# Performance work log

Hardware: AMD Instinct MI355X
Metric: run time of the kernel (lower is better)

Reference implementation:

```python
import jax, jax.numpy as jnp
import numpy as np

H = 128        # hidden_size == embed dim
HEADS = 8
HD = H // HEADS  # 16
OUT = 2


def _mlp(x, w1, b1, w2, b2, w3, b3):
    # build_mlps(2, [128, 64, 128], ret_before_act=True, without_norm=True)
    x = jax.nn.relu(x @ w1.T + b1)
    x = jax.nn.relu(x @ w2.T + b2)
    return x @ w3.T + b3


def _cross_attn(q, kv, mask, wq, bq, wk, bk, wv, bv, wo, bo):
    # q: [B, A, H] agent queries; kv: [B, M, H] map polylines; mask: [B, M] True = padded
    B, A, _ = q.shape
    M = kv.shape[1]
    qh = (q @ wq.T + bq).reshape(B, A, HEADS, HD)
    kh = (kv @ wk.T + bk).reshape(B, M, HEADS, HD)
    vh = (kv @ wv.T + bv).reshape(B, M, HEADS, HD)
    scores = jnp.einsum('bahd,bmhd->bham', qh, kh) * (1.0 / np.sqrt(HD))
    scores = jnp.where(mask[:, None, None, :], jnp.finfo(scores.dtype).min, scores)
    attn = jax.nn.softmax(scores, axis=-1)
    out = jnp.einsum('bham,bmhd->bahd', attn, vh).reshape(B, A, H)
    return out @ wo.T + bo


def _lstm_cell(x, h, c, avail, w_ih, w_hh, b_ih, b_hh):
    # standard torch LSTMCell math, masked update per agent availability
    gates = x @ w_ih.T + b_ih + h @ w_hh.T + b_hh
    i, f, g, o = jnp.split(gates, 4, axis=-1)
    c_new = jax.nn.sigmoid(f) * c + jax.nn.sigmoid(i) * jnp.tanh(g)
    h_new = jax.nn.sigmoid(o) * jnp.tanh(c_new)
    m = avail[..., None]
    return jnp.where(m, h_new, h), jnp.where(m, c_new, c)


def setup_inputs() -> dict:
    key = jax.random.key(0)
    B, A, M, T = 128, 64, 512, 80
    ks = jax.random.split(key, 32)
    p = lambda k, shape: (jax.random.normal(k, shape, dtype=jnp.float32) * 0.02)
    map_avails = jax.random.uniform(ks[5], (B, M)) > 0.2
    map_avails = map_avails.at[:, :8].set(True)  # guarantee non-empty attention rows
    return {
        'current_features': jax.random.normal(ks[0], (B, A, 2), dtype=jnp.float32),
        'current_availabilities': jnp.ones((B, A), dtype=bool),
        'hidden': jax.random.normal(ks[1], (B, A, H), dtype=jnp.float32),
        'context': jax.random.normal(ks[2], (B, A, H), dtype=jnp.float32),
        'map_embedding': jax.random.normal(ks[3], (B, M, H), dtype=jnp.float32),
        'map_avails': map_avails,
        'n_timesteps': T,
        # state encoder MLP: 2 -> 128 -> 64 -> 128
        'enc_w1': p(ks[6], (128, 2)),  'enc_b1': jnp.zeros((128,), jnp.float32),
        'enc_w2': p(ks[7], (64, 128)), 'enc_b2': jnp.zeros((64,), jnp.float32),
        'enc_w3': p(ks[8], (128, 64)), 'enc_b3': jnp.zeros((128,), jnp.float32),
        # cross-attention projections
        'wq': p(ks[9], (H, H)),  'bq': jnp.zeros((H,), jnp.float32),
        'wk': p(ks[10], (H, H)), 'bk': jnp.zeros((H,), jnp.float32),
        'wv': p(ks[11], (H, H)), 'bv': jnp.zeros((H,), jnp.float32),
        'wo': p(ks[12], (H, H)), 'bo': jnp.zeros((H,), jnp.float32),
        # LSTM cell (input 128, hidden 128)
        'w_ih': p(ks[13], (4 * H, H)), 'w_hh': p(ks[14], (4 * H, H)),
        'b_ih': jnp.zeros((4 * H,), jnp.float32), 'b_hh': jnp.zeros((4 * H,), jnp.float32),
        # output head
        'lin_w': p(ks[15], (OUT, H)), 'lin_b': jnp.zeros((OUT,), jnp.float32),
    }


def reference(current_features, current_availabilities, hidden, context,
              map_embedding, map_avails, n_timesteps,
              enc_w1, enc_b1, enc_w2, enc_b2, enc_w3, enc_b3,
              wq, bq, wk, bk, wv, bv, wo, bo,
              w_ih, w_hh, b_ih, b_hh, lin_w, lin_b):
    state0 = current_features[..., :2]
    cross_mask = ~map_avails

    def step(carry, _):
        state, h, c = carry
        e = _mlp(state, enc_w1, enc_b1, enc_w2, enc_b2, enc_w3, enc_b3)
        e = _cross_attn(e, map_embedding, cross_mask, wq, bq, wk, bk, wv, bv, wo, bo)
        h, c = _lstm_cell(e, h, c, current_availabilities, w_ih, w_hh, b_ih, b_hh)
        state = state + h @ lin_w.T + lin_b
        return (state, h, c), state

    _, ys = jax.lax.scan(step, (state0, hidden, context), None, length=n_timesteps)
    return jnp.moveaxis(ys, 0, 2)  # [B, A, T, 2]
```

## Files before the change

kernel.cpp:

```cpp
#include <hip/hip_runtime.h>
#include <cstdint>
#include <cstddef>


typedef short short8 __attribute__((ext_vector_type(8)));
typedef float f32x4 __attribute__((ext_vector_type(4)));

#define LOG2E 1.4426950408889634f
#define QSCALE 0.36067376022224085f

__device__ __forceinline__ unsigned short f2bf(float f) {
  union { float f; unsigned int u; } v; v.f = f;
  unsigned int u = v.u;
  return (unsigned short)((u + 0x7fffu + ((u >> 16) & 1u)) >> 16);
}
__device__ __forceinline__ unsigned cvtpk_bf16(float lo, float hi) {
  unsigned r;
  asm("v_cvt_pk_bf16_f32 %0, %1, %2" : "=v"(r) : "v"(lo), "v"(hi));
  return r;
}
__device__ __forceinline__ float fexp2(float x) {
  return __builtin_amdgcn_exp2f(x);
}
__device__ __forceinline__ float frcp(float x) {
  return __builtin_amdgcn_rcpf(x);
}
__device__ __forceinline__ float sigm(float x) {
  return frcp(1.f + fexp2(-LOG2E * x));
}
__device__ __forceinline__ float tanh_f(float x) {
  return 1.f - 2.f * frcp(1.f + fexp2(2.f * LOG2E * x));
}
__device__ __forceinline__ f32x4 splat4(float v) { f32x4 r = {v, v, v, v}; return r; }
__device__ __forceinline__ unsigned char f2fp8(float x) {
  return (unsigned char)__builtin_amdgcn_cvt_pk_fp8_f32(x, x, 0, false);
}
__device__ __forceinline__ f32x4 mfma_fp8(long a, long b, f32x4 c) {
  return __builtin_amdgcn_mfma_f32_16x16x32_fp8_fp8(a, b, c, 0, 0, 0);
}
__device__ __forceinline__ f32x4 mfma_bf16(short8 a, short8 b, f32x4 c) {
  return __builtin_amdgcn_mfma_f32_16x16x32_bf16(a, b, c, 0, 0, 0);
}

__global__ __launch_bounds__(256) void prep_kernel(
    const float* __restrict__ emb, const float* __restrict__ wk,
    const float* __restrict__ bk, const float* __restrict__ wv,
    const float* __restrict__ bv,
    const float* __restrict__ w2, const float* __restrict__ whh,
    const float* __restrict__ wih, const float* __restrict__ wo,
    const float* __restrict__ wq, const float* __restrict__ w3,
    const float* __restrict__ b3, const float* __restrict__ bq,
    const float* __restrict__ bo, const float* __restrict__ bih,
    const float* __restrict__ bhh,
    unsigned char* __restrict__ K8, unsigned char* __restrict__ V8,
    unsigned short* __restrict__ W2, unsigned short* __restrict__ WHH,
    unsigned short* __restrict__ WIHO, unsigned short* __restrict__ WQ3,
    float* __restrict__ B4p, float* __restrict__ BQ3S) {
  extern __shared__ char smem[];
  const int tid = threadIdx.x;
  const int blk = blockIdx.x;

  if (blk < 1024) {
    unsigned short* s_e = (unsigned short*)smem;
    unsigned short* s_wk = (unsigned short*)(smem + 17408);
    unsigned short* s_wv = (unsigned short*)(smem + 52224);
    const int b = blk >> 3;
    const int m0 = (blk & 7) * 64;
    const int wave = tid >> 6;
    const int lane = tid & 63;
    const int quad = lane >> 4;
    const int l16 = lane & 15;

    for (int i = tid; i < 4096; i += 256) {
      int j = i * 2, row = j >> 7, col = j & 127;
      const float* p = emb + (size_t)(b * 512 + m0 + row) * 128 + col;
      *(unsigned*)(s_e + row * 136 + col) = cvtpk_bf16(p[0], p[1]);
    }
    for (int i = tid; i < 8192; i += 256) {
      int j = i * 2, row = j >> 7, col = j & 127;
      *(unsigned*)(s_wk + row * 136 + col) =
          cvtpk_bf16(wk[row * 128 + col], wk[row * 128 + col + 1]);
      *(unsigned*)(s_wv + row * 136 + col) =
          cvtpk_bf16(wv[row * 128 + col], wv[row * 128 + col + 1]);
    }
    __syncthreads();

    {
      const int mt = wave;
      short8 a8[4];
#pragma unroll
      for (int kt = 0; kt < 4; ++kt)
        a8[kt] = *(const short8*)(s_e + (mt * 16 + l16) * 136 + kt * 32 + quad * 8);
#pragma unroll
      for (int nt = 0; nt < 8; ++nt) {
        f32x4 acc = {0.f, 0.f, 0.f, 0.f};
#pragma unroll
        for (int kt = 0; kt < 4; ++kt) {
          short8 b8 = *(const short8*)(s_wk + (nt * 16 + l16) * 136 + kt * 32 + quad * 8);
          acc = mfma_bf16(a8[kt], b8, acc);
        }
        const int d = nt * 16 + l16;
        const float bkd = bk[d];
#pragma unroll
        for (int r = 0; r < 4; ++r)
          K8[(size_t)(b * 512 + m0 + mt * 16 + quad * 4 + r) * 128 + d] =
              f2fp8(acc[r] + bkd);
      }
    }
    {
      const int dt0 = wave * 2;
#pragma unroll
      for (int dt = dt0; dt < dt0 + 2; ++dt) {
        short8 a8[4];
#pragma unroll
        for (int kt = 0; kt < 4; ++kt)
          a8[kt] = *(const short8*)(s_wv + (dt * 16 + l16) * 136 + kt * 32 + quad * 8);
#pragma unroll
        for (int nt = 0; nt < 4; ++nt) {
          f32x4 acc = {0.f, 0.f, 0.f, 0.f};
#pragma unroll
          for (int kt = 0; kt < 4; ++kt) {
            short8 b8 = *(const short8*)(s_e + (nt * 16 + l16) * 136 + kt * 32 + quad * 8);
            acc = mfma_bf16(a8[kt], b8, acc);
          }
          const int m = m0 + nt * 16 + l16;
          const int ml = m & 31;
          const int sperm = (ml < 16) ? (((ml >> 2) << 3) | (ml & 3))
                                      : ((((ml - 16) >> 2) << 3) | ((ml - 16) & 3) | 4);
          const int mpos = (m & ~31) | sperm;
#pragma unroll
          for (int r = 0; r < 4; ++r) {
            const int d = dt * 16 + quad * 4 + r;
            V8[(size_t)(b * 128 + d) * 512 + mpos] = f2fp8(acc[r] + bv[d]);
          }
        }
      }
    }
  } else if (blk < 1280) {
    int i = (blk - 1024) * 256 + tid;
    int r = i >> 7, d = i & 127;
    float acc = 0.f;
    for (int n = 0; n < 128; ++n)
      acc = fmaf(wih[r * 128 + n], wo[n * 128 + d], acc);
    WIHO[i] = f2bf(acc);
  } else if (blk < 1568) {
    int i = (blk - 1280) * 256 + tid;
    if (i < 8192) W2[i] = f2bf(w2[i]);
    else if (i < 73728) WHH[i - 8192] = f2bf(whh[i - 8192]);
  } else {
    int i = (blk - 1568) * 256 + tid;
    if (i < 8192) {
      int n = i >> 6, k = i & 63;
      float acc = 0.f;
      for (int j = 0; j < 128; ++j) acc = fmaf(wq[n * 128 + j], w3[j * 64 + k], acc);
      WQ3[i] = f2bf(acc * QSCALE);
    } else if (i < 8704) {
      int r = i - 8192;
      float acc = bih[r] + bhh[r];
      for (int n = 0; n < 128; ++n) acc = fmaf(wih[r * 128 + n], bo[n], acc);
      B4p[r] = acc;
    } else if (i < 8832) {
      int n = i - 8704;
      float acc = bq[n];
      for (int j = 0; j < 128; ++j) acc = fmaf(wq[n * 128 + j], b3[j], acc);
      BQ3S[n] = acc * QSCALE;
    }
  }
}

__global__ __launch_bounds__(512, 2) void decoder_kernel(
    const float* __restrict__ cf, const int* __restrict__ cav,
    const float* __restrict__ hid,
    const float* __restrict__ ctx, const int* __restrict__ mav,
    const int* __restrict__ ntp,
    const float* __restrict__ w1, const float* __restrict__ b1,
    const float* __restrict__ b2,
    const unsigned char* __restrict__ K8, const unsigned char* __restrict__ V8,
    const unsigned short* __restrict__ W2, const unsigned short* __restrict__ WQ3,
    const unsigned short* __restrict__ WIHO, const unsigned short* __restrict__ WHH,
    const float* __restrict__ B4p, const float* __restrict__ BQ3S,
    const float* __restrict__ lnw, const float* __restrict__ lnb,
    float* __restrict__ out) {
  extern __shared__ char smem[];
  unsigned short* s_bufA = (unsigned short*)(smem + 131072);
  unsigned short* s_bufB = (unsigned short*)(smem + 139776);
  unsigned short* s_h = (unsigned short*)(smem + 148480);
  unsigned short* s_h2 = (unsigned short*)(smem + 157184);
  unsigned char* s_maskb = (unsigned char*)(smem + 162048);

  const int tid = threadIdx.x;
  const int wave = tid >> 6;
  const int lane = tid & 63;
  const int quad = lane >> 4;
  const int l16 = lane & 15;

  const int b = blockIdx.x & 127;
  const int a0 = (blockIdx.x >> 7) * 32;
  const int T = *ntp;
  const f32x4 zero4 = {0.f, 0.f, 0.f, 0.f};
  const long kOnes = 0x3838383838383838L;

  {
    const unsigned long long* Kg = (const unsigned long long*)(K8 + (size_t)b * 65536);
    for (int i = tid; i < 8192; i += 512) {
      int tok = i >> 4, seg = i & 15;
      *(unsigned long long*)(smem + tok * 128 + ((seg * 8) ^ ((tok & 15) * 8))) =
          Kg[(size_t)tok * 16 + seg];
    }
    const unsigned long long* Vg = (const unsigned long long*)(V8 + (size_t)b * 65536);
    for (int i = tid; i < 8192; i += 512) {
      int d = i >> 6, seg = i & 63;
      *(unsigned long long*)(smem + 65536 + d * 512 + ((seg * 8) ^ ((d & 15) * 8))) =
          Vg[(size_t)d * 64 + seg];
    }
  }
  s_maskb[tid] = mav[b * 512 + tid] ? 1 : 0;
  {
    int idx = tid * 8;
    int a = idx >> 7, n0 = idx & 127;
    const float* hp = hid + (size_t)(b * 64 + a0 + a) * 128 + n0;
    short8 v;
#pragma unroll
    for (int j = 0; j < 8; ++j) v[j] = (short)f2bf(hp[j]);
    *(short8*)(s_h + a * 136 + n0) = v;
  }
  float c_reg[2][4], avl[2][4];
#pragma unroll
  for (int mt = 0; mt < 2; ++mt)
#pragma unroll
    for (int r = 0; r < 4; ++r) {
      int a = mt * 16 + quad * 4 + r;
      c_reg[mt][r] = ctx[(size_t)(b * 64 + a0 + a) * 128 + wave * 16 + l16];
      avl[mt][r] = (cav[b * 64 + a0 + a] != 0) ? 1.f : 0.f;
    }

  const int wrow = wave * 16 + l16;
  short8 rIH[4][4], rHH[4][4];
#pragma unroll
  for (int kt = 0; kt < 4; ++kt)
#pragma unroll
    for (int g = 0; g < 4; ++g) {
      rIH[kt][g] = *(const short8*)(WIHO + ((g * 128 + wrow) * 128 + kt * 32 + quad * 8));
      rHH[kt][g] = *(const short8*)(WHH + ((g * 128 + wrow) * 128 + kt * 32 + quad * 8));
    }
  short8 rWQ3[2];
#pragma unroll
  for (int kt = 0; kt < 2; ++kt)
    rWQ3[kt] = *(const short8*)(WQ3 + (wrow * 64 + kt * 32 + quad * 8));
  float rB4[4];
#pragma unroll
  for (int g = 0; g < 4; ++g) rB4[g] = B4p[g * 128 + wrow];
  const float rBQ3 = BQ3S[wrow];
  const float rB2 = b2[(wave & 3) * 16 + l16];

  const int p7_o = tid >> 3, p7_sub = tid & 7;
  const int p7_a = p7_o >> 1, p7_oi = p7_o & 1;
  const float mylnb = lnb[p7_oi];
  float myst = cf[(size_t)(b * 64 + a0 + p7_a) * 2 + p7_oi];

  __syncthreads();

  unsigned mflags = 0;
#pragma unroll
  for (int i = 0; i < 32; ++i)
    if (!s_maskb[i * 16 + l16]) mflags |= (1u << i);

  {
    float other = __shfl_xor(myst, 8);
    float st0 = p7_oi ? other : myst;
    float st1 = p7_oi ? myst : other;
    int a = tid >> 4, n0 = (tid & 15) * 8;
    const float* wp = w1 + n0 * 2;
    const float* bp = b1 + n0;
    float x[8];
#pragma unroll
    for (int j = 0; j < 8; ++j)
      x[j] = fmaxf(fmaf(wp[j * 2], st0, fmaf(wp[j * 2 + 1], st1, bp[j])), 0.f);
    union { short8 s; unsigned u[4]; } v;
#pragma unroll
    for (int j = 0; j < 4; ++j) v.u[j] = cvtpk_bf16(x[j * 2], x[j * 2 + 1]);
    *(short8*)(s_bufA + a * 136 + n0) = v.s;
  }
  __syncthreads();

#pragma unroll 1
  for (int t = 0; t < T; ++t) {
    {
      int mt = wave >> 2, nt = wave & 3;
      f32x4 acc = splat4(rB2);
#pragma unroll
      for (int kt = 0; kt < 4; ++kt) {
        short8 a8 = *(const short8*)(s_bufA + (mt * 16 + l16) * 136 + kt * 32 + quad * 8);
        short8 b8 = *(const short8*)(W2 + ((nt * 16 + l16) * 128 + kt * 32 + quad * 8));
        acc = mfma_bf16(a8, b8, acc);
      }
      unsigned pk01 = cvtpk_bf16(fmaxf(acc[0], 0.f), fmaxf(acc[1], 0.f));
      unsigned pk23 = cvtpk_bf16(fmaxf(acc[2], 0.f), fmaxf(acc[3], 0.f));
      unsigned short* hb = s_h2 + (mt * 16 + quad * 4) * 72 + nt * 16 + l16;
      hb[0] = (unsigned short)pk01;
      hb[72] = (unsigned short)(pk01 >> 16);
      hb[144] = (unsigned short)pk23;
      hb[216] = (unsigned short)(pk23 >> 16);
    }
    __syncthreads();

    unsigned char* s_q8 = (unsigned char*)s_bufA;
    {
#pragma unroll
      for (int mt = 0; mt < 2; ++mt) {
        f32x4 acc = splat4(rBQ3);
#pragma unroll
        for (int kt = 0; kt < 2; ++kt) {
          short8 a8 = *(const short8*)(s_h2 + (mt * 16 + l16) * 72 + kt * 32 + quad * 8);
          acc = mfma_bf16(a8, rWQ3[kt], acc);
        }
#pragma unroll
        for (int r = 0; r < 4; ++r)
          s_q8[(mt * 16 + quad * 4 + r) * 136 + wave * 16 + l16] = f2fp8(acc[r]);
      }
    }
    __asm__ volatile("s_waitcnt lgkmcnt(0)" ::: "memory");
    __builtin_amdgcn_sched_barrier(0);

    {
      const int h = wave;
      const char* sKb = (const char*)smem;
      const char* sVrow = (const char*)(smem + 65536) + (h * 16 + l16) * 512;
      long qA[2];
#pragma unroll
      for (int mt = 0; mt < 2; ++mt)
        qA[mt] = (quad < 2)
                     ? *(const long*)(s_q8 + (mt * 16 + l16) * 136 + h * 16 + quad * 8)
                     : (quad == 2 ? 0xF8L : 0L);
      const int koff = (h * 16 + quad * 8) ^ (l16 * 8);
      f32x4 O[2], L4[2];
      O[0] = zero4; O[1] = zero4; L4[0] = zero4; L4[1] = zero4;
      long vA_c = *(const long*)(sVrow + ((quad * 8) ^ (l16 * 8)));
      long kB_c0 = 0L, kB_c1 = 0L;
      if (quad < 2) {
        kB_c0 = *(const long*)(sKb + (size_t)l16 * 128 + koff);
        kB_c1 = *(const long*)(sKb + (size_t)(16 + l16) * 128 + koff);
      }
#pragma unroll 4
      for (int c = 0; c < 16; ++c) {
        long vA_n = 0L, kB_n0 = 0L, kB_n1 = 0L;
        if (c < 15) {
          vA_n = *(const long*)(sVrow + (((c + 1) * 32 + quad * 8) ^ (l16 * 8)));
          if (quad < 2) {
            kB_n0 = *(const long*)(sKb + (size_t)((c + 1) * 32 + l16) * 128 + koff);
            kB_n1 = *(const long*)(sKb + (size_t)((c + 1) * 32 + 16 + l16) * 128 + koff);
          }
        }
        long kB0 = kB_c0, kB1 = kB_c1;
        if (quad == 2) {
          kB0 = ((mflags >> (c * 2)) & 1u) ? 0x38L : 0L;
          kB1 = ((mflags >> (c * 2 + 1)) & 1u) ? 0x38L : 0L;
        }
        __builtin_amdgcn_s_setprio(1);
        f32x4 S2[2][2];
        S2[0][0] = mfma_fp8(kB0, qA[0], zero4);
        S2[0][1] = mfma_fp8(kB0, qA[1], zero4);
        S2[1][0] = mfma_fp8(kB1, qA[0], zero4);
        S2[1][1] = mfma_fp8(kB1, qA[1], zero4);
        __builtin_amdgcn_s_setprio(0);
        long pB[2];
#pragma unroll
        for (int mt = 0; mt < 2; ++mt) {
          unsigned w0 = (unsigned)__builtin_amdgcn_cvt_pk_fp8_f32(
              fexp2(S2[0][mt][0]), fexp2(S2[0][mt][1]), 0, false);
          w0 = (unsigned)__builtin_amdgcn_cvt_pk_fp8_f32(
              fexp2(S2[0][mt][2]), fexp2(S2[0][mt][3]), (int)w0, true);
          unsigned w1v = (unsigned)__builtin_amdgcn_cvt_pk_fp8_f32(
              fexp2(S2[1][mt][0]), fexp2(S2[1][mt][1]), 0, false);
          w1v = (unsigned)__builtin_amdgcn_cvt_pk_fp8_f32(
              fexp2(S2[1][mt][2]), fexp2(S2[1][mt][3]), (int)w1v, true);
          pB[mt] = (long)(((unsigned long long)w1v << 32) | (unsigned long long)w0);
        }
        __builtin_amdgcn_s_setprio(1);
        O[0] = mfma_fp8(vA_c, pB[0], O[0]);
        L4[0] = mfma_fp8(kOnes, pB[0], L4[0]);
        O[1] = mfma_fp8(vA_c, pB[1], O[1]);
        L4[1] = mfma_fp8(kOnes, pB[1], L4[1]);
        __builtin_amdgcn_s_setprio(0);
        vA_c = vA_n; kB_c0 = kB_n0; kB_c1 = kB_n1;
      }
#pragma unroll
      for (int mt = 0; mt < 2; ++mt) {
        float o0 = O[mt][0] * frcp(L4[mt][0]);
        float o1 = O[mt][1] * frcp(L4[mt][1]);
        float o2 = O[mt][2] * frcp(L4[mt][2]);
        float o3 = O[mt][3] * frcp(L4[mt][3]);
        unsigned long long ow =
            ((unsigned long long)cvtpk_bf16(o2, o3) << 32) | cvtpk_bf16(o0, o1);
        *(unsigned long long*)(s_bufB + (mt * 16 + l16) * 136 + h * 16 + quad * 4) = ow;
      }
    }
    __syncthreads();

    {
      const int ni = wave;
      f32x4 gi[2], gf[2], gg[2], go[2];
#pragma unroll
      for (int mt = 0; mt < 2; ++mt) {
        gi[mt] = splat4(rB4[0]);
        gf[mt] = splat4(rB4[1]);
        gg[mt] = splat4(rB4[2]);
        go[mt] = splat4(rB4[3]);
      }
      __builtin_amdgcn_s_setprio(1);
#pragma unroll
      for (int kt = 0; kt < 4; ++kt)
#pragma unroll
        for (int mt = 0; mt < 2; ++mt) {
          short8 a8 = *(const short8*)(s_bufB + (mt * 16 + l16) * 136 + kt * 32 + quad * 8);
          gi[mt] = mfma_bf16(a8, rIH[kt][0], gi[mt]);
          gf[mt] = mfma_bf16(a8, rIH[kt][1], gf[mt]);
          gg[mt] = mfma_bf16(a8, rIH[kt][2], gg[mt]);
          go[mt] = mfma_bf16(a8, rIH[kt][3], go[mt]);
        }
#pragma unroll
      for (int kt = 0; kt < 4; ++kt)
#pragma unroll
        for (int mt = 0; mt < 2; ++mt) {
          short8 a8 = *(const short8*)(s_h + (mt * 16 + l16) * 136 + kt * 32 + quad * 8);
          gi[mt] = mfma_bf16(a8, rHH[kt][0], gi[mt]);
          gf[mt] = mfma_bf16(a8, rHH[kt][1], gf[mt]);
          gg[mt] = mfma_bf16(a8, rHH[kt][2], gg[mt]);
          go[mt] = mfma_bf16(a8, rHH[kt][3], go[mt]);
        }
      __builtin_amdgcn_s_setprio(0);
      float hnew[2][4];
#pragma unroll
      for (int mt = 0; mt < 2; ++mt)
#pragma unroll
        for (int r = 0; r < 4; ++r) {
          float iv = sigm(gi[mt][r]);
          float fv = sigm(gf[mt][r]);
          float gv = tanh_f(gg[mt][r]);
          float ov = sigm(go[mt][r]);
          float cn = fmaf(fv, c_reg[mt][r], iv * gv);
          float hv = ov * tanh_f(cn);
          int arow = mt * 16 + quad * 4 + r;
          float av = avl[mt][r];
          union { unsigned int u; float f; } ho;
          ho.u = ((unsigned int)s_h[arow * 136 + ni * 16 + l16]) << 16;
          c_reg[mt][r] = av * cn + (1.f - av) * c_reg[mt][r];
          hnew[mt][r] = av * hv + (1.f - av) * ho.f;
        }
      __syncthreads();
#pragma unroll
      for (int mt = 0; mt < 2; ++mt)
#pragma unroll
        for (int r = 0; r < 4; ++r) {
          int arow = mt * 16 + quad * 4 + r;
          s_h[arow * 136 + ni * 16 + l16] = f2bf(hnew[mt][r]);
        }
    }
    __syncthreads();

    {
      const unsigned short* hp = s_h + p7_a * 136 + p7_sub * 16;
      const float* lw = lnw + p7_oi * 128 + p7_sub * 16;
      short8 h0 = *(const short8*)hp;
      short8 h1 = *(const short8*)(hp + 8);
      float acc = 0.f;
#pragma unroll
      for (int k = 0; k < 8; ++k) {
        union { unsigned int u; float f; } hv;
        hv.u = ((unsigned int)(unsigned short)h0[k]) << 16;
        acc = fmaf(hv.f, lw[k], acc);
      }
#pragma unroll
      for (int k = 0; k < 8; ++k) {
        union { unsigned int u; float f; } hv;
        hv.u = ((unsigned int)(unsigned short)h1[k]) << 16;
        acc = fmaf(hv.f, lw[8 + k], acc);
      }
      acc += __shfl_xor(acc, 4);
      acc += __shfl_xor(acc, 2);
      acc += __shfl_xor(acc, 1);
      float ns = myst + acc + mylnb;
      myst = ns;
      if (p7_sub == 0)
        out[((size_t)(b * 64 + a0 + p7_a) * T + t) * 2 + p7_oi] = ns;
      float other = __shfl_xor(ns, 8);
      float st0 = p7_oi ? other : ns;
      float st1 = p7_oi ? ns : other;
      int a = tid >> 4, n0 = (tid & 15) * 8;
      const float* wp = w1 + n0 * 2;
      const float* bp = b1 + n0;
      float x[8];
#pragma unroll
      for (int j = 0; j < 8; ++j)
        x[j] = fmaxf(fmaf(wp[j * 2], st0, fmaf(wp[j * 2 + 1], st1, bp[j])), 0.f);
      union { short8 s; unsigned u[4]; } v;
#pragma unroll
      for (int j = 0; j < 4; ++j) v.u[j] = cvtpk_bf16(x[j * 2], x[j * 2 + 1]);
      *(short8*)(s_bufA + a * 136 + n0) = v.s;
    }
    __syncthreads();
  }
}

extern "C" void kernel_launch(void* const* d_in, const int* in_sizes, int n_in,
                              void* d_out, int out_size, void* d_ws, size_t ws_size,
                              hipStream_t stream) {
  (void)in_sizes; (void)n_in; (void)out_size; (void)ws_size;
  const float* cf = (const float*)d_in[0];
  const int* cav = (const int*)d_in[1];
  const float* hid = (const float*)d_in[2];
  const float* ctx = (const float*)d_in[3];
  const float* emb = (const float*)d_in[4];
  const int* mav = (const int*)d_in[5];
  const int* ntp = (const int*)d_in[6];
  const float* w1 = (const float*)d_in[7];
  const float* b1 = (const float*)d_in[8];
  const float* w2 = (const float*)d_in[9];
  const float* b2 = (const float*)d_in[10];
  const float* w3 = (const float*)d_in[11];
  const float* b3 = (const float*)d_in[12];
  const float* wq = (const float*)d_in[13];
  const float* bq = (const float*)d_in[14];
  const float* wk = (const float*)d_in[15];
  const float* bk = (const float*)d_in[16];
  const float* wv = (const float*)d_in[17];
  const float* bv = (const float*)d_in[18];
  const float* wo = (const float*)d_in[19];
  const float* bo = (const float*)d_in[20];
  const float* wih = (const float*)d_in[21];
  const float* whh = (const float*)d_in[22];
  const float* bih = (const float*)d_in[23];
  const float* bhh = (const float*)d_in[24];
  const float* lnw = (const float*)d_in[25];
  const float* lnb = (const float*)d_in[26];

  char* ws = (char*)d_ws;
  unsigned char* K8 = (unsigned char*)(ws + 0);
  unsigned char* V8 = (unsigned char*)(ws + 8388608);
  unsigned short* W2s = (unsigned short*)(ws + 16777216);
  unsigned short* WQ3s = (unsigned short*)(ws + 16793600);
  unsigned short* WIHOs = (unsigned short*)(ws + 16809984);
  unsigned short* WHHs = (unsigned short*)(ws + 16941056);
  float* B4p = (float*)(ws + 17072128);
  float* BQ3S = (float*)(ws + 17074176);

  (void)hipFuncSetAttribute((const void*)prep_kernel,
                            hipFuncAttributeMaxDynamicSharedMemorySize, 87040);
  (void)hipFuncSetAttribute((const void*)decoder_kernel,
                            hipFuncAttributeMaxDynamicSharedMemorySize, 162560);

  prep_kernel<<<1603, 256, 87040, stream>>>(
      emb, wk, bk, wv, bv, w2, whh, wih, wo, wq, w3, b3, bq, bo, bih, bhh,
      K8, V8, W2s, WHHs, WIHOs, WQ3s, B4p, BQ3S);
  decoder_kernel<<<256, 512, 162560, stream>>>(
      cf, cav, hid, ctx, mav, ntp, w1, b1, b2, K8, V8, W2s, WQ3s, WIHOs, WHHs,
      B4p, BQ3S, lnw, lnb, (float*)d_out);
}
```

Measured before the change: 1.117 ms.

## Ping-pong hidden-state buffers to drop a barrier; shrink prep LDS

```diff
diff --git a/kernel.cpp b/kernel.cpp
--- a/kernel.cpp
+++ b/kernel.cpp
@@ -62,8 +62,7 @@
 
   if (blk < 1024) {
     unsigned short* s_e = (unsigned short*)smem;
-    unsigned short* s_wk = (unsigned short*)(smem + 17408);
-    unsigned short* s_wv = (unsigned short*)(smem + 52224);
+    unsigned short* s_w = (unsigned short*)(smem + 17408);
     const int b = blk >> 3;
     const int m0 = (blk & 7) * 64;
     const int wave = tid >> 6;
@@ -78,10 +77,8 @@
     }
     for (int i = tid; i < 8192; i += 256) {
       int j = i * 2, row = j >> 7, col = j & 127;
-      *(unsigned*)(s_wk + row * 136 + col) =
+      *(unsigned*)(s_w + row * 136 + col) =
           cvtpk_bf16(wk[row * 128 + col], wk[row * 128 + col + 1]);
-      *(unsigned*)(s_wv + row * 136 + col) =
-          cvtpk_bf16(wv[row * 128 + col], wv[row * 128 + col + 1]);
     }
     __syncthreads();
 
@@ -96,7 +93,7 @@
         f32x4 acc = {0.f, 0.f, 0.f, 0.f};
 #pragma unroll
         for (int kt = 0; kt < 4; ++kt) {
-          short8 b8 = *(const short8*)(s_wk + (nt * 16 + l16) * 136 + kt * 32 + quad * 8);
+          short8 b8 = *(const short8*)(s_w + (nt * 16 + l16) * 136 + kt * 32 + quad * 8);
           acc = mfma_bf16(a8[kt], b8, acc);
         }
         const int d = nt * 16 + l16;
@@ -107,6 +104,13 @@
               f2fp8(acc[r] + bkd);
       }
     }
+    __syncthreads();
+    for (int i = tid; i < 8192; i += 256) {
+      int j = i * 2, row = j >> 7, col = j & 127;
+      *(unsigned*)(s_w + row * 136 + col) =
+          cvtpk_bf16(wv[row * 128 + col], wv[row * 128 + col + 1]);
+    }
+    __syncthreads();
     {
       const int dt0 = wave * 2;
 #pragma unroll
@@ -114,7 +118,7 @@
         short8 a8[4];
 #pragma unroll
         for (int kt = 0; kt < 4; ++kt)
-          a8[kt] = *(const short8*)(s_wv + (dt * 16 + l16) * 136 + kt * 32 + quad * 8);
+          a8[kt] = *(const short8*)(s_w + (dt * 16 + l16) * 136 + kt * 32 + quad * 8);
 #pragma unroll
         for (int nt = 0; nt < 4; ++nt) {
           f32x4 acc = {0.f, 0.f, 0.f, 0.f};
@@ -182,9 +186,9 @@
     const float* __restrict__ lnw, const float* __restrict__ lnb,
     float* __restrict__ out) {
   extern __shared__ char smem[];
-  unsigned short* s_bufA = (unsigned short*)(smem + 131072);
+  unsigned short* s_bufV = (unsigned short*)(smem + 131072);
   unsigned short* s_bufB = (unsigned short*)(smem + 139776);
-  unsigned short* s_h = (unsigned short*)(smem + 148480);
+  unsigned short* s_bufU = (unsigned short*)(smem + 148480);
   unsigned short* s_h2 = (unsigned short*)(smem + 157184);
   unsigned char* s_maskb = (unsigned char*)(smem + 162048);
 
@@ -222,7 +226,7 @@
     short8 v;
 #pragma unroll
     for (int j = 0; j < 8; ++j) v[j] = (short)f2bf(hp[j]);
-    *(short8*)(s_h + a * 136 + n0) = v;
+    *(short8*)(s_bufU + a * 136 + n0) = v;
   }
   float c_reg[2][4], avl[2][4];
 #pragma unroll
@@ -279,32 +283,35 @@
     union { short8 s; unsigned u[4]; } v;
 #pragma unroll
     for (int j = 0; j < 4; ++j) v.u[j] = cvtpk_bf16(x[j * 2], x[j * 2 + 1]);
-    *(short8*)(s_bufA + a * 136 + n0) = v.s;
+    *(short8*)(s_bufV + a * 136 + n0) = v.s;
   }
   __syncthreads();
 
 #pragma unroll 1
   for (int t = 0; t < T; ++t) {
+    unsigned short* hb = (t & 1) ? s_bufV : s_bufU;
+    unsigned short* xb = (t & 1) ? s_bufU : s_bufV;
+
     {
       int mt = wave >> 2, nt = wave & 3;
       f32x4 acc = splat4(rB2);
 #pragma unroll
       for (int kt = 0; kt < 4; ++kt) {
-        short8 a8 = *(const short8*)(s_bufA + (mt * 16 + l16) * 136 + kt * 32 + quad * 8);
+        short8 a8 = *(const short8*)(xb + (mt * 16 + l16) * 136 + kt * 32 + quad * 8);
         short8 b8 = *(const short8*)(W2 + ((nt * 16 + l16) * 128 + kt * 32 + quad * 8));
         acc = mfma_bf16(a8, b8, acc);
       }
       unsigned pk01 = cvtpk_bf16(fmaxf(acc[0], 0.f), fmaxf(acc[1], 0.f));
       unsigned pk23 = cvtpk_bf16(fmaxf(acc[2], 0.f), fmaxf(acc[3], 0.f));
-      unsigned short* hb = s_h2 + (mt * 16 + quad * 4) * 72 + nt * 16 + l16;
-      hb[0] = (unsigned short)pk01;
-      hb[72] = (unsigned short)(pk01 >> 16);
-      hb[144] = (unsigned short)pk23;
-      hb[216] = (unsigned short)(pk23 >> 16);
-    }
-    __syncthreads();
-
-    unsigned char* s_q8 = (unsigned char*)s_bufA;
+      unsigned short* hbp = s_h2 + (mt * 16 + quad * 4) * 72 + nt * 16 + l16;
+      hbp[0] = (unsigned short)pk01;
+      hbp[72] = (unsigned short)(pk01 >> 16);
+      hbp[144] = (unsigned short)pk23;
+      hbp[216] = (unsigned short)(pk23 >> 16);
+    }
+    __syncthreads();
+
+    unsigned char* s_q8 = (unsigned char*)xb;
     {
 #pragma unroll
       for (int mt = 0; mt < 2; ++mt) {
@@ -422,14 +429,13 @@
       for (int kt = 0; kt < 4; ++kt)
 #pragma unroll
         for (int mt = 0; mt < 2; ++mt) {
-          short8 a8 = *(const short8*)(s_h + (mt * 16 + l16) * 136 + kt * 32 + quad * 8);
+          short8 a8 = *(const short8*)(hb + (mt * 16 + l16) * 136 + kt * 32 + quad * 8);
           gi[mt] = mfma_bf16(a8, rHH[kt][0], gi[mt]);
           gf[mt] = mfma_bf16(a8, rHH[kt][1], gf[mt]);
           gg[mt] = mfma_bf16(a8, rHH[kt][2], gg[mt]);
           go[mt] = mfma_bf16(a8, rHH[kt][3], go[mt]);
         }
       __builtin_amdgcn_s_setprio(0);
-      float hnew[2][4];
 #pragma unroll
       for (int mt = 0; mt < 2; ++mt)
 #pragma unroll
@@ -443,23 +449,16 @@
           int arow = mt * 16 + quad * 4 + r;
           float av = avl[mt][r];
           union { unsigned int u; float f; } ho;
-          ho.u = ((unsigned int)s_h[arow * 136 + ni * 16 + l16]) << 16;
+          ho.u = ((unsigned int)hb[arow * 136 + ni * 16 + l16]) << 16;
           c_reg[mt][r] = av * cn + (1.f - av) * c_reg[mt][r];
-          hnew[mt][r] = av * hv + (1.f - av) * ho.f;
-        }
-      __syncthreads();
-#pragma unroll
-      for (int mt = 0; mt < 2; ++mt)
-#pragma unroll
-        for (int r = 0; r < 4; ++r) {
-          int arow = mt * 16 + quad * 4 + r;
-          s_h[arow * 136 + ni * 16 + l16] = f2bf(hnew[mt][r]);
-        }
-    }
-    __syncthreads();
-
-    {
-      const unsigned short* hp = s_h + p7_a * 136 + p7_sub * 16;
+          float hn = av * hv + (1.f - av) * ho.f;
+          xb[arow * 136 + ni * 16 + l16] = f2bf(hn);
+        }
+    }
+    __syncthreads();
+
+    {
+      const unsigned short* hp = xb + p7_a * 136 + p7_sub * 16;
       const float* lw = lnw + p7_oi * 128 + p7_sub * 16;
       short8 h0 = *(const short8*)hp;
       short8 h1 = *(const short8*)(hp + 8);
@@ -496,7 +495,7 @@
       union { short8 s; unsigned u[4]; } v;
 #pragma unroll
       for (int j = 0; j < 4; ++j) v.u[j] = cvtpk_bf16(x[j * 2], x[j * 2 + 1]);
-      *(short8*)(s_bufA + a * 136 + n0) = v.s;
+      *(short8*)(hb + a * 136 + n0) = v.s;
     }
     __syncthreads();
   }
@@ -545,11 +544,11 @@
   float* BQ3S = (float*)(ws + 17074176);
 
   (void)hipFuncSetAttribute((const void*)prep_kernel,
-                            hipFuncAttributeMaxDynamicSharedMemorySize, 87040);
+                            hipFuncAttributeMaxDynamicSharedMemorySize, 52224);
   (void)hipFuncSetAttribute((const void*)decoder_kernel,
                             hipFuncAttributeMaxDynamicSharedMemorySize, 162560);
 
-  prep_kernel<<<1603, 256, 87040, stream>>>(
+  prep_kernel<<<1603, 256, 52224, stream>>>(
       emb, wk, bk, wv, bv, w2, whh, wih, wo, wq, w3, b3, bq, bo, bih, bhh,
       K8, V8, W2s, WHHs, WIHOs, WQ3s, B4p, BQ3S);
   decoder_kernel<<<256, 512, 162560, stream>>>(
```

Measured after the change: 1.091 ms. 2.3% less time.
